# Kernel tuning notes

Measured on AMD Instinct MI355X. Metric: run time of the kernel, lower is better.

Reference implementation:

```python
import jax, jax.numpy as jnp
import numpy as np

LANDMARKS = 80
POINT_LANDMARKS = tuple(range(468, 538))  # 70 hand-region indices
AVG_SET = [[0,40],[40,40],[80,60],[140,60],[200,60],[260,60],[320,50],[370,50],[420,60],[480,63]]
STAT_CAP = 168


def nan_mean(x, axis=0):
    m = jnp.isnan(x)
    num = jnp.where(m, 0.0, x).sum(axis)
    den = jnp.where(m, 0.0, 1.0).sum(axis)
    return num / den


def nan_std(x, axis=0):
    d = x - nan_mean(x, axis=axis)
    return jnp.sqrt(nan_mean(d * d, axis=axis))


def flatten_means_and_stds(x, reshape1):
    # x: [t, L, C] -> stats over frames -> [2L, C] -> (1, reshape1*2)
    out = jnp.concatenate([nan_mean(x, 0), nan_std(x, 0)], axis=0)
    if out.shape[0] > STAT_CAP:
        out = out[:STAT_CAP, :]
    out = out.reshape(1, reshape1 * 2)
    return jnp.where(jnp.isfinite(out), out, jnp.zeros_like(out))


def setup_inputs() -> dict:
    key = jax.random.key(0)
    T, N, C = 32768, 543, 3
    x_in = jax.random.normal(key, (T, N, C), dtype=jnp.float32)
    return {
        "x_in": x_in,
        "num_frames": 16384,
        "segments": 4,
        "input_shape": (16384, 240),
    }


def reference(x_in, num_frames, segments, input_shape):
    # 1) cluster means + point gather -> x: [T, LANDMARKS, 3]
    parts = [jnp.mean(x_in[:, s:s + l, :], axis=1, keepdims=True) for s, l in AVG_SET]
    parts.append(x_in[:, jnp.array(POINT_LANDMARKS), :])
    x = jnp.concatenate(parts, axis=1)

    # 2) symmetric padding loop (axis 1), gated on T % segments as in the original
    xp = x
    rem = x.shape[0] % segments  # shapes are static -> Python int
    for i in range(segments):
        p0 = 1 if (rem > 0 and i % 2 != 0) else 0
        p1 = 1 if (rem > 0 and i % 2 == 0) else 0
        if p0 or p1:
            xp = jnp.pad(xp, ((0, 0), (p0, p1), (0, 0)), mode='symmetric')

    # 3) per-segment nan mean/std stats
    segs = np.array_split(np.arange(xp.shape[0]), segments)
    feats = [flatten_means_and_stds(xp[idx[0]:idx[-1] + 1], input_shape[1]) for idx in segs]
    feats.append(flatten_means_and_stds(x, input_shape[1]))

    # 4) bilinear resize (align_corners=False semantics, no antialias)
    xi = jnp.transpose(x, (2, 0, 1))[None]            # [1, 3, T, L]
    xi = jax.image.resize(xi, (1, 3, num_frames, LANDMARKS), method='bilinear', antialias=False)
    xi = jnp.transpose(xi[0], (1, 2, 0))              # [num_frames, L, 3]
    xi = xi.reshape(1, input_shape[0] * input_shape[1])
    xi = jnp.where(jnp.isnan(xi), jnp.zeros_like(xi), xi)
    feats.append(xi)

    return jnp.concatenate(feats, axis=1)
```

## Files before the change

kernel.cpp:

```cpp
#include <hip/hip_runtime.h>
#include <math.h>

#define T_FRAMES   32768
#define N_LM       543
#define FRAME      1629
#define FPB        32
#define NBLOCKS    (T_FRAMES / FPB)
#define OUT_B_OFF  2400
#define ACC_FLOATS 1920

__constant__ int   c_astart[10] = {0, 40, 80, 140, 200, 260, 320, 370, 420, 480};
__constant__ int   c_alen[10]   = {40, 40, 60, 60, 60, 60, 50, 50, 60, 63};

__global__ void zero_acc_kernel(float* __restrict__ acc) {
    int i = blockIdx.x * 256 + threadIdx.x;
    if (i < ACC_FLOATS) acc[i] = 0.0f;
}

__global__ __launch_bounds__(256) void featgen_main(
    const float* __restrict__ xin, float* __restrict__ out, float* __restrict__ acc)
{
    __shared__ float rows[4 * FRAME];
    __shared__ float xavg[4 * 32];

    const int t = threadIdx.x;
    const int b = blockIdx.x;
    const float* src = xin + (size_t)b * (FPB * FRAME);

    const int g8 = t >> 3;
    const int j8 = t & 7;
    int a_s = 0, a_n = 0, a_c = 0;
    float a_inv = 0.0f;
    if (g8 < 30) {
        int l = g8 / 3; a_c = g8 - 3 * l;
        a_s = c_astart[l]; a_n = c_alen[l];
        a_inv = 1.0f / (float)a_n;
    }

    float ssum = 0.0f, ssq = 0.0f;

    for (int grp = 0; grp < 8; ++grp) {
        const float4* s4 = (const float4*)(src + grp * (4 * FRAME));
        float4* d4 = (float4*)rows;
        #pragma unroll
        for (int i = 0; i < 7; ++i) {
            int idx = t + i * 256;
            if (idx < FRAME) d4[idx] = s4[idx];
        }
        __syncthreads();

        if (g8 < 30) {
            #pragma unroll
            for (int f = 0; f < 4; ++f) {
                const float* row = rows + f * FRAME;
                float s = 0.0f;
                for (int j = j8; j < a_n; j += 8) s += row[(a_s + j) * 3 + a_c];
                s += __shfl_xor(s, 1, 8);
                s += __shfl_xor(s, 2, 8);
                s += __shfl_xor(s, 4, 8);
                if (j8 == 0) xavg[f * 32 + g8] = s * a_inv;
            }
        }
        __syncthreads();

        if (t < 240) {
            float v0, v1, v2, v3;
            if (t < 30) {
                v0 = xavg[0 * 32 + t]; v1 = xavg[1 * 32 + t];
                v2 = xavg[2 * 32 + t]; v3 = xavg[3 * 32 + t];
            } else {
                v0 = rows[0 * FRAME + t + 1374];
                v1 = rows[1 * FRAME + t + 1374];
                v2 = rows[2 * FRAME + t + 1374];
                v3 = rows[3 * FRAME + t + 1374];
            }
            const size_t row0 = (size_t)b * 16 + (size_t)grp * 2;
            out[OUT_B_OFF + row0 * 240 + t]       = 0.5f * (v0 + v1);
            out[OUT_B_OFF + (row0 + 1) * 240 + t] = 0.5f * (v2 + v3);
            ssum += v0 + v1 + v2 + v3;
            ssq  += v0 * v0 + v1 * v1 + v2 * v2 + v3 * v3;
        }
        __syncthreads();
    }

    if (t < 240) {
        const int seg = b >> 8;
        atomicAdd(&acc[seg * 480 + t],       ssum);
        atomicAdd(&acc[seg * 480 + 240 + t], ssq);
    }
}

__global__ __launch_bounds__(256) void finalize_stats(
    const float* __restrict__ acc, float* __restrict__ out)
{
    const int f = blockIdx.x;
    const int t = threadIdx.x;
    if (t >= 240) return;
    float s, q, n;
    if (f < 4) {
        s = acc[f * 480 + t];
        q = acc[f * 480 + 240 + t];
        n = 8192.0f;
    } else {
        s = acc[t]       + acc[480 + t]  + acc[960 + t]  + acc[1440 + t];
        q = acc[240 + t] + acc[720 + t]  + acc[1200 + t] + acc[1680 + t];
        n = 32768.0f;
    }
    float mean = s / n;
    float var  = q / n - mean * mean;
    var = var < 0.0f ? 0.0f : var;
    out[f * 480 + t]       = mean;
    out[f * 480 + 240 + t] = sqrtf(var);
}

extern "C" void kernel_launch(void* const* d_in, const int* in_sizes, int n_in,
                              void* d_out, int out_size, void* d_ws, size_t ws_size,
                              hipStream_t stream) {
    (void)in_sizes; (void)n_in; (void)out_size; (void)ws_size;
    const float* xin = (const float*)d_in[0];
    float* out = (float*)d_out;
    float* acc = (float*)d_ws;

    zero_acc_kernel<<<8, 256, 0, stream>>>(acc);
    featgen_main<<<NBLOCKS, 256, 0, stream>>>(xin, out, acc);
    finalize_stats<<<5, 256, 0, stream>>>(acc, out);
}
```

Measured before the change: 307.8 us.

## Register-prefetch next tile, halve frames per block, drop xavg shared staging

Each block now handles 16 frames instead of 32, doubling the grid, and sets a minimum-occupancy launch bound. The next 4-frame tile is prefetched into registers while the current tile is processed, then written to shared memory. Cluster averages are written straight from the reducing lanes instead of being staged through a shared xavg array, which removes one barrier per tile. The cost is extra registers for the prefetch buffer and twice as many atomic adds into the accumulators.

```diff
diff --git a/kernel.cpp b/kernel.cpp
--- a/kernel.cpp
+++ b/kernel.cpp
@@ -4,8 +4,10 @@
 #define T_FRAMES   32768
 #define N_LM       543
 #define FRAME      1629
-#define FPB        32
+#define FPB        16
 #define NBLOCKS    (T_FRAMES / FPB)
+#define TILES      4
+#define TILE_F4    1629
 #define OUT_B_OFF  2400
 #define ACC_FLOATS 1920
 
@@ -17,11 +19,10 @@
     if (i < ACC_FLOATS) acc[i] = 0.0f;
 }
 
-__global__ __launch_bounds__(256) void featgen_main(
+__global__ __launch_bounds__(256, 6) void featgen_main(
     const float* __restrict__ xin, float* __restrict__ out, float* __restrict__ acc)
 {
     __shared__ float rows[4 * FRAME];
-    __shared__ float xavg[4 * 32];
 
     const int t = threadIdx.x;
     const int b = blockIdx.x;
@@ -38,18 +39,40 @@
     }
 
     float ssum = 0.0f, ssq = 0.0f;
+    float lsum = 0.0f, lsq = 0.0f;
 
-    for (int grp = 0; grp < 8; ++grp) {
-        const float4* s4 = (const float4*)(src + grp * (4 * FRAME));
+    float4 pre[7];
+
+    {
+        const float4* s4 = (const float4*)src;
+        #pragma unroll
+        for (int i = 0; i < 7; ++i) {
+            int idx = t + i * 256;
+            if (idx < TILE_F4) pre[i] = s4[idx];
+        }
         float4* d4 = (float4*)rows;
         #pragma unroll
         for (int i = 0; i < 7; ++i) {
             int idx = t + i * 256;
-            if (idx < FRAME) d4[idx] = s4[idx];
+            if (idx < TILE_F4) d4[idx] = pre[i];
         }
-        __syncthreads();
+    }
+    __syncthreads();
+
+    for (int grp = 0; grp < TILES; ++grp) {
+        if (grp < TILES - 1) {
+            const float4* s4 = (const float4*)(src + (size_t)(grp + 1) * (4 * FRAME));
+            #pragma unroll
+            for (int i = 0; i < 7; ++i) {
+                int idx = t + i * 256;
+                if (idx < TILE_F4) pre[i] = s4[idx];
+            }
+        }
+
+        const size_t row0 = (size_t)b * (FPB / 2) + (size_t)grp * 2;
 
         if (g8 < 30) {
+            float v[4];
             #pragma unroll
             for (int f = 0; f < 4; ++f) {
                 const float* row = rows + f * FRAME;
@@ -58,33 +81,46 @@
                 s += __shfl_xor(s, 1, 8);
                 s += __shfl_xor(s, 2, 8);
                 s += __shfl_xor(s, 4, 8);
-                if (j8 == 0) xavg[f * 32 + g8] = s * a_inv;
+                v[f] = s * a_inv;
+            }
+            if (j8 == 0) {
+                out[OUT_B_OFF + row0 * 240 + g8]       = 0.5f * (v[0] + v[1]);
+                out[OUT_B_OFF + (row0 + 1) * 240 + g8] = 0.5f * (v[2] + v[3]);
+                lsum += v[0] + v[1] + v[2] + v[3];
+                lsq  += v[0]*v[0] + v[1]*v[1] + v[2]*v[2] + v[3]*v[3];
             }
         }
-        __syncthreads();
 
-        if (t < 240) {
-            float v0, v1, v2, v3;
-            if (t < 30) {
-                v0 = xavg[0 * 32 + t]; v1 = xavg[1 * 32 + t];
-                v2 = xavg[2 * 32 + t]; v3 = xavg[3 * 32 + t];
-            } else {
-                v0 = rows[0 * FRAME + t + 1374];
-                v1 = rows[1 * FRAME + t + 1374];
-                v2 = rows[2 * FRAME + t + 1374];
-                v3 = rows[3 * FRAME + t + 1374];
-            }
-            const size_t row0 = (size_t)b * 16 + (size_t)grp * 2;
+        if (t >= 30 && t < 240) {
+            float v0 = rows[0 * FRAME + t + 1374];
+            float v1 = rows[1 * FRAME + t + 1374];
+            float v2 = rows[2 * FRAME + t + 1374];
+            float v3 = rows[3 * FRAME + t + 1374];
             out[OUT_B_OFF + row0 * 240 + t]       = 0.5f * (v0 + v1);
             out[OUT_B_OFF + (row0 + 1) * 240 + t] = 0.5f * (v2 + v3);
             ssum += v0 + v1 + v2 + v3;
-            ssq  += v0 * v0 + v1 * v1 + v2 * v2 + v3 * v3;
+            ssq  += v0*v0 + v1*v1 + v2*v2 + v3*v3;
         }
+
         __syncthreads();
+
+        if (grp < TILES - 1) {
+            float4* d4 = (float4*)rows;
+            #pragma unroll
+            for (int i = 0; i < 7; ++i) {
+                int idx = t + i * 256;
+                if (idx < TILE_F4) d4[idx] = pre[i];
+            }
+            __syncthreads();
+        }
     }
 
-    if (t < 240) {
-        const int seg = b >> 8;
+    const int seg = b >> 9;
+    if (g8 < 30 && j8 == 0) {
+        atomicAdd(&acc[seg * 480 + g8],       lsum);
+        atomicAdd(&acc[seg * 480 + 240 + g8], lsq);
+    }
+    if (t >= 30 && t < 240) {
         atomicAdd(&acc[seg * 480 + t],       ssum);
         atomicAdd(&acc[seg * 480 + 240 + t], ssq);
     }
```

New measurement: 375.4 us. 1.22x slower.
